# Optimization experiments

Hardware: AMD Instinct MI355X
Metric: run time of the kernel (lower is better)

## Reference

```python
import jax, jax.numpy as jnp
import numpy as np

B, T, C, L = 256, 512, 256, 64
NEG = -1e30  # log-space 'zero'
BLANK = 0


def setup_inputs() -> dict:
    key = jax.random.key(0)
    k1, k2, k3, k4 = jax.random.split(key, 4)
    logits = jax.random.normal(k1, (B, T, C), dtype=jnp.float32)
    targets = jax.random.randint(k2, (B, L), 1, C)            # labels never equal blank (0)
    input_lengths = jax.random.randint(k3, (B,), T - 100, T + 1)
    target_lengths = jax.random.randint(k4, (B,), L // 2, L + 1)
    return dict(logits=logits, targets=targets,
                input_lengths=input_lengths, target_lengths=target_lengths)


def _ctc_loss(logits, targets, input_lengths, target_lengths):
    Bb, Tt, Cc = logits.shape
    Ll = targets.shape[1]
    S = 2 * Ll + 1  # extended label length (blanks interleaved)

    # fused log_softmax over vocab (original does permute then log_softmax; same math)
    logp = jax.nn.log_softmax(logits, axis=-1)  # [B,T,C]

    # extended target sequence: blank, y1, blank, y2, ..., blank
    ext = jnp.zeros((Bb, S), jnp.int32).at[:, 1::2].set(targets.astype(jnp.int32))
    # gather log-probs of extended labels for every timestep: [B,T,S]
    lp_ext = jnp.take_along_axis(logp, jnp.broadcast_to(ext[:, None, :], (Bb, Tt, S)), axis=2)

    # skip transition s-2 -> s allowed iff ext[s] != blank and ext[s] != ext[s-2]
    skip = jnp.zeros((Bb, S), bool).at[:, 2:].set(
        (ext[:, 2:] != BLANK) & (ext[:, 2:] != ext[:, :-2]))

    # alpha at t=0
    alpha0 = (jnp.full((Bb, S), NEG, dtype=logits.dtype)
              .at[:, 0].set(lp_ext[:, 0, 0])
              .at[:, 1].set(lp_ext[:, 0, 1]))

    neg1 = jnp.full((Bb, 1), NEG, dtype=logits.dtype)
    neg2 = jnp.full((Bb, 2), NEG, dtype=logits.dtype)

    def step(alpha, inputs):
        lp_t, t = inputs  # lp_t: [B,S]
        a1 = alpha
        a2 = jnp.concatenate([neg1, alpha[:, :-1]], axis=1)
        a3 = jnp.where(skip, jnp.concatenate([neg2, alpha[:, :-2]], axis=1), NEG)
        new = jnp.logaddexp(jnp.logaddexp(a1, a2), a3) + lp_t
        new = jnp.maximum(new, NEG)  # keep impossible paths bounded
        # freeze alpha for batch rows whose input sequence already ended
        alpha = jnp.where((t < input_lengths)[:, None], new, alpha)
        return alpha, None

    ts = jnp.arange(1, Tt)
    alphaT, _ = jax.lax.scan(step, alpha0, (jnp.swapaxes(lp_ext, 0, 1)[1:], ts))

    tl = target_lengths.astype(jnp.int32)
    a_last = jnp.take_along_axis(alphaT, (2 * tl)[:, None], axis=1)[:, 0]
    a_prev = jnp.take_along_axis(alphaT, (2 * tl - 1)[:, None], axis=1)[:, 0]
    loss = -jnp.logaddexp(a_last, a_prev)            # [B]
    loss = jnp.where(loss > 1e20, 0.0, loss)          # zero_infinity=True
    # reduction='mean': per-sample loss divided by target length, then batch mean
    return (loss / tl.astype(loss.dtype)).mean()


def reference(logits, targets, input_lengths, target_lengths):
    return _ctc_loss(logits, targets, input_lengths, target_lengths)
```

## Files before the change

### kernel.cpp

```cpp
#include <hip/hip_runtime.h>

#define B_ 256
#define T_ 512
#define C_ 256
#define L_ 64
#define S_ 129
#define TCH 64
#define LOG2E 1.44269504f
#define LN2 0.69314718f

template <int CTRL>
__device__ __forceinline__ int dpp_mov_i32(int x) {
    return __builtin_amdgcn_update_dpp(0, x, CTRL, 0xF, 0xF, true);
}

__device__ __forceinline__ double shr1d(double x) {
    int2 u = __builtin_bit_cast(int2, x);
    u.x = dpp_mov_i32<0x138>(u.x);
    u.y = dpp_mov_i32<0x138>(u.y);
    return __builtin_bit_cast(double, u);
}

template <int CTRL>
__device__ __forceinline__ double dpp_mov_f64(double x) {
    int2 u = __builtin_bit_cast(int2, x);
    u.x = dpp_mov_i32<CTRL>(u.x);
    u.y = dpp_mov_i32<CTRL>(u.y);
    return __builtin_bit_cast(double, u);
}

__device__ __forceinline__ float wave_sum(float x) {
#define DPPADD(ctrl)                                                          \
    x += __builtin_bit_cast(float, dpp_mov_i32<ctrl>(__builtin_bit_cast(int, x)));
    DPPADD(0x111) DPPADD(0x112) DPPADD(0x114)
    DPPADD(0x118) DPPADD(0x142) DPPADD(0x143)
#undef DPPADD
    return __builtin_bit_cast(float,
        __builtin_amdgcn_readlane(__builtin_bit_cast(int, x), 63));
}

__device__ __forceinline__ double wave_max_d(double x) {
    x = fmax(x, dpp_mov_f64<0x111>(x));
    x = fmax(x, dpp_mov_f64<0x112>(x));
    x = fmax(x, dpp_mov_f64<0x114>(x));
    x = fmax(x, dpp_mov_f64<0x118>(x));
    x = fmax(x, dpp_mov_f64<0x142>(x));
    x = fmax(x, dpp_mov_f64<0x143>(x));
    int2 u = __builtin_bit_cast(int2, x);
    u.x = __builtin_amdgcn_readlane(u.x, 63);
    u.y = __builtin_amdgcn_readlane(u.y, 63);
    return __builtin_bit_cast(double, u);
}

__device__ __forceinline__ void rescale(double& a0, double& a1, double& a2, int& e) {
    const double m = wave_max_d(fmax(fmax(a0, a1), a2));
    const int hi = __builtin_bit_cast(int2, m).y;
    int ex = ((hi >> 20) & 0x7ff) - 1023;
    if (m == 0.0) ex = 0;
    e += ex;
    int2 fb; fb.x = 0; fb.y = (1023 - ex) << 20;
    const double f = __builtin_bit_cast(double, fb);
    a0 *= f; a1 *= f; a2 *= f;
}

__device__ __forceinline__ float log2_pos(double a) {
    if (a == 0.0) return -1e30f;
    int2 u = __builtin_bit_cast(int2, a);
    const int ex = ((u.y >> 20) & 0x7ff) - 1023;
    u.y = (u.y & 0x800FFFFF) | (1023 << 20);
    const float mf = (float)__builtin_bit_cast(double, u);
    return __log2f(mf) + (float)ex;
}

__global__ __launch_bounds__(576) void k_fused(const float* __restrict__ logits,
                                               const int* __restrict__ targets,
                                               const int* __restrict__ in_len,
                                               const int* __restrict__ tg_len,
                                               float* __restrict__ out) {
    const int b = blockIdx.x;
    const int w = threadIdx.x >> 6;
    const int l = threadIdx.x & 63;

    __shared__ float2 P[2][TCH][64];
    __shared__ float4 rb4[8][2][64];
    __shared__ int   tgt_sh[L_];
    __shared__ float alpha_sh[S_];
    __shared__ int   prod_done;
    __shared__ int   cons_done;

    if (threadIdx.x == 0) { prod_done = 0; cons_done = 0; }
    if (threadIdx.x < L_) tgt_sh[threadIdx.x] = targets[(b << 6) + threadIdx.x];
    __syncthreads();

    const int len = in_len[b];
    const size_t rowbase = (size_t)b * T_;

    if (w > 0) {
        const int mytgt = tgt_sh[l];
        const int tt0 = (w - 1) * 8;
        float4 va[8], vb[8];
        #pragma unroll
        for (int r = 0; r < 8; ++r)
            va[r] = ((const float4*)logits)[(rowbase + tt0 + r) * 64 + l];

        for (int k = 0; k < 8; ++k) {
            if (k < 7) {
                #pragma unroll
                for (int r = 0; r < 8; ++r) {
                    const int t = (k + 1) * TCH + tt0 + r;
                    vb[r] = ((const float4*)logits)[(rowbase + t) * 64 + l];
                }
            }
            if (k >= 2) {
                while (__hip_atomic_load(&cons_done, __ATOMIC_ACQUIRE,
                                         __HIP_MEMORY_SCOPE_WORKGROUP) < k - 1) {}
            }
            #pragma unroll
            for (int r = 0; r < 8; ++r) {
                const int tt = tt0 + r;
                float4 e;
                e.x = exp2f(va[r].x * LOG2E);
                e.y = exp2f(va[r].y * LOG2E);
                e.z = exp2f(va[r].z * LOG2E);
                e.w = exp2f(va[r].w * LOG2E);
                rb4[w - 1][r & 1][l] = e;
                const float stot = wave_sum(e.x + e.y + e.z + e.w);
                const float rs = __builtin_amdgcn_rcpf(stot);
                const float eb = __builtin_bit_cast(float,
                    __builtin_amdgcn_readfirstlane(__builtin_bit_cast(int, e.x)));
                const float eo = ((const float*)&rb4[w - 1][r & 1][0])[mytgt];
                float2 pq; pq.x = eb * rs; pq.y = eo * rs;
                P[k & 1][tt][l] = pq;
            }
            if (l == 0)
                __hip_atomic_fetch_add(&prod_done, 1, __ATOMIC_RELEASE,
                                       __HIP_MEMORY_SCOPE_WORKGROUP);
            #pragma unroll
            for (int r = 0; r < 8; ++r) va[r] = vb[r];
        }
        return;
    }

    __builtin_amdgcn_s_setprio(1);
    const int tc = tgt_sh[l];
    const int tp = __shfl_up(tc, 1);
    const bool skip = (l >= 1) && (tc != tp);
    const int tl = tg_len[b];

    double a0 = 0.0, a1 = 0.0, a2 = 0.0;
    int scale_total = 0;

    for (int k = 0; k < 8; ++k) {
        while (__hip_atomic_load(&prod_done, __ATOMIC_ACQUIRE,
                                 __HIP_MEMORY_SCOPE_WORKGROUP) < 8 * (k + 1)) {}
        const int kb = k & 1;
        const int base = k * TCH;
        float2 pa[8], pn[8];
        #pragma unroll
        for (int j = 0; j < 8; ++j) pa[j] = P[kb][j][l];
        if (k == 0) {
            a0 = (l == 0) ? (double)pa[0].x : 0.0;
            a1 = (l == 0) ? (double)pa[0].y : 0.0;
            a2 = 0.0;
        }
        for (int g = 0; g < 8; ++g) {
            if (g < 7) {
                #pragma unroll
                for (int j = 0; j < 8; ++j) pn[j] = P[kb][(g + 1) * 8 + j][l];
            }
            #pragma unroll
            for (int j = 0; j < 8; ++j) {
                const int t = base + g * 8 + j;
                if (t >= 1 && t < len) {
                    const double p = shr1d(a1);
                    const double c = skip ? p : 0.0;
                    const double a0n = (a0 + p) * (double)pa[j].x;
                    const double a1n = ((a1 + a0) + c) * (double)pa[j].y;
                    const double a2n = (a2 + a1) * (double)pa[j].x;
                    a0 = a0n; a1 = a1n; a2 = a2n;
                }
            }
            if (g == 3 || g == 7) rescale(a0, a1, a2, scale_total);
            if (g < 7) {
                #pragma unroll
                for (int j = 0; j < 8; ++j) pa[j] = pn[j];
            }
        }
        if (l == 0)
            __hip_atomic_fetch_add(&cons_done, 1, __ATOMIC_RELEASE,
                                   __HIP_MEMORY_SCOPE_WORKGROUP);
    }

    alpha_sh[2 * l]     = log2_pos(a0);
    alpha_sh[2 * l + 1] = log2_pos(a1);
    if (l == 63) alpha_sh[128] = log2_pos(a2);
    if (l == 0) {
        const float al = alpha_sh[2 * tl];
        const float ap = alpha_sh[2 * tl - 1];
        const float m  = fmaxf(al, ap);
        const float lse2 = m + __log2f(exp2f(al - m) + exp2f(ap - m));
        float loss = -LN2 * (lse2 + (float)scale_total);
        if (!(loss < 1e20f)) loss = 0.0f;
        atomicAdd(out, loss / (float)tl * (1.0f / (float)B_));
    }
}

extern "C" void kernel_launch(void* const* d_in, const int* in_sizes, int n_in,
                              void* d_out, int out_size, void* d_ws, size_t ws_size,
                              hipStream_t stream) {
    const float* logits  = (const float*)d_in[0];
    const int*   targets = (const int*)d_in[1];
    const int*   in_len  = (const int*)d_in[2];
    const int*   tg_len  = (const int*)d_in[3];
    float*       out     = (float*)d_out;

    (void)hipMemsetAsync(d_out, 0, sizeof(float), stream);
    k_fused<<<B_, 576, 0, stream>>>(logits, targets, in_len, tg_len, out);
}
```

Measured before the change: 203.3 us.

## Triple-buffer producer/consumer ring and tighten the alpha recurrence inner loop

Grows the shared-memory probability ring from two chunk buffers to three, so the producer waves can run one more chunk ahead of the single consumer wave. Spin-waits now call s_sleep to reduce LDS polling pressure. The consumer's recurrence carries the pairwise sums (a0+a1, a1+a2) from step to step to shorten the dependent add chain. It also replaces the per-step length predicate with whole-group fast paths plus a tail loop. The larger ring costs more LDS per block, and the sleeps may add wake-up latency on the critical consumer path.

```diff
diff --git a/kernel.cpp b/kernel.cpp
--- a/kernel.cpp
+++ b/kernel.cpp
@@ -6,6 +6,7 @@
 #define L_ 64
 #define S_ 129
 #define TCH 64
+#define NRING 3
 #define LOG2E 1.44269504f
 #define LN2 0.69314718f
 
@@ -81,7 +82,7 @@
     const int w = threadIdx.x >> 6;
     const int l = threadIdx.x & 63;
 
-    __shared__ float2 P[2][TCH][64];
+    __shared__ float2 P[NRING][TCH][64];
     __shared__ float4 rb4[8][2][64];
     __shared__ int   tgt_sh[L_];
     __shared__ float alpha_sh[S_];
@@ -103,6 +104,7 @@
         for (int r = 0; r < 8; ++r)
             va[r] = ((const float4*)logits)[(rowbase + tt0 + r) * 64 + l];
 
+        int kb = 0;
         for (int k = 0; k < 8; ++k) {
             if (k < 7) {
                 #pragma unroll
@@ -111,9 +113,10 @@
                     vb[r] = ((const float4*)logits)[(rowbase + t) * 64 + l];
                 }
             }
-            if (k >= 2) {
+            if (k >= NRING) {
                 while (__hip_atomic_load(&cons_done, __ATOMIC_ACQUIRE,
-                                         __HIP_MEMORY_SCOPE_WORKGROUP) < k - 1) {}
+                                         __HIP_MEMORY_SCOPE_WORKGROUP) < k - (NRING - 1))
+                    __builtin_amdgcn_s_sleep(2);
             }
             #pragma unroll
             for (int r = 0; r < 8; ++r) {
@@ -130,13 +133,14 @@
                     __builtin_amdgcn_readfirstlane(__builtin_bit_cast(int, e.x)));
                 const float eo = ((const float*)&rb4[w - 1][r & 1][0])[mytgt];
                 float2 pq; pq.x = eb * rs; pq.y = eo * rs;
-                P[k & 1][tt][l] = pq;
+                P[kb][tt][l] = pq;
             }
             if (l == 0)
                 __hip_atomic_fetch_add(&prod_done, 1, __ATOMIC_RELEASE,
                                        __HIP_MEMORY_SCOPE_WORKGROUP);
             #pragma unroll
             for (int r = 0; r < 8; ++r) va[r] = vb[r];
+            if (++kb == NRING) kb = 0;
         }
         return;
     }
@@ -147,49 +151,64 @@
     const bool skip = (l >= 1) && (tc != tp);
     const int tl = tg_len[b];
 
-    double a0 = 0.0, a1 = 0.0, a2 = 0.0;
+    double a0 = 0.0, a1 = 0.0, a2 = 0.0, s01 = 0.0, s12 = 0.0;
     int scale_total = 0;
 
+#define STEP(pb, po)                                                          \
+    {                                                                         \
+        const double p = shr1d(a1);                                           \
+        const double c = skip ? p : 0.0;                                      \
+        const double a0n = (a0 + p) * (pb);                                   \
+        const double a1n = (s01 + c) * (po);                                  \
+        const double a2n = s12 * (pb);                                        \
+        a0 = a0n; a1 = a1n; a2 = a2n;                                         \
+        s01 = a1n + a0n; s12 = a2n + a1n;                                     \
+    }
+
+    int kb = 0;
     for (int k = 0; k < 8; ++k) {
         while (__hip_atomic_load(&prod_done, __ATOMIC_ACQUIRE,
-                                 __HIP_MEMORY_SCOPE_WORKGROUP) < 8 * (k + 1)) {}
-        const int kb = k & 1;
+                                 __HIP_MEMORY_SCOPE_WORKGROUP) < 8 * (k + 1))
+            __builtin_amdgcn_s_sleep(2);
         const int base = k * TCH;
-        float2 pa[8], pn[8];
-        #pragma unroll
-        for (int j = 0; j < 8; ++j) pa[j] = P[kb][j][l];
-        if (k == 0) {
-            a0 = (l == 0) ? (double)pa[0].x : 0.0;
-            a1 = (l == 0) ? (double)pa[0].y : 0.0;
-            a2 = 0.0;
-        }
+        const int rem  = len - base;
+        const int lim  = rem > TCH ? TCH : (rem < 0 ? 0 : rem);
+
         for (int g = 0; g < 8; ++g) {
-            if (g < 7) {
+            const int gb = g * 8;
+            float2 pa[8];
+            #pragma unroll
+            for (int j = 0; j < 8; ++j) pa[j] = P[kb][gb + j][l];
+            double pbd[8], pod[8];
+            #pragma unroll
+            for (int j = 0; j < 8; ++j) {
+                pbd[j] = (double)pa[j].x;
+                pod[j] = (double)pa[j].y;
+            }
+            if (k == 0 && g == 0) {
+                a0 = (l == 0) ? pbd[0] : 0.0;
+                a1 = (l == 0) ? pod[0] : 0.0;
+                a2 = 0.0; s01 = a0 + a1; s12 = a1;
                 #pragma unroll
-                for (int j = 0; j < 8; ++j) pn[j] = P[kb][(g + 1) * 8 + j][l];
-            }
-            #pragma unroll
-            for (int j = 0; j < 8; ++j) {
-                const int t = base + g * 8 + j;
-                if (t >= 1 && t < len) {
-                    const double p = shr1d(a1);
-                    const double c = skip ? p : 0.0;
-                    const double a0n = (a0 + p) * (double)pa[j].x;
-                    const double a1n = ((a1 + a0) + c) * (double)pa[j].y;
-                    const double a2n = (a2 + a1) * (double)pa[j].x;
-                    a0 = a0n; a1 = a1n; a2 = a2n;
-                }
-            }
-            if (g == 3 || g == 7) rescale(a0, a1, a2, scale_total);
-            if (g < 7) {
+                for (int j = 1; j < 8; ++j) STEP(pbd[j], pod[j])
+            } else if (gb + 8 <= lim) {
                 #pragma unroll
-                for (int j = 0; j < 8; ++j) pa[j] = pn[j];
+                for (int j = 0; j < 8; ++j) STEP(pbd[j], pod[j])
+            } else if (gb < lim) {
+                const int cnt = lim - gb;
+                for (int j = 0; j < cnt; ++j) STEP(pbd[j], pod[j])
+            }
+            if (g == 3 || g == 7) {
+                rescale(a0, a1, a2, scale_total);
+                s01 = a1 + a0; s12 = a2 + a1;
             }
         }
         if (l == 0)
             __hip_atomic_fetch_add(&cons_done, 1, __ATOMIC_RELEASE,
                                    __HIP_MEMORY_SCOPE_WORKGROUP);
-    }
+        if (++kb == NRING) kb = 0;
+    }
+#undef STEP
 
     alpha_sh[2 * l]     = log2_pos(a0);
     alpha_sh[2 * l + 1] = log2_pos(a1);
```

Result: no change. 202.1 us (-0.5%).
